# Performance work log

Hardware: AMD Instinct MI355X
Metric: run time of the kernel (lower is better)

Reference implementation:

```python
import jax, jax.numpy as jnp
import numpy as np


def setup_inputs() -> dict:
    key = jax.random.key(0)
    ks = jax.random.split(key, 13)
    B, W, C = 16, 2048, 512
    inp = {
        "X_sfr": jax.random.normal(ks[0], (B, W, C), dtype=jnp.float32),
        "adj_matrix": jax.random.normal(ks[1], (B, C, C), dtype=jnp.float32),
        "log_temp": jnp.zeros((1,), dtype=jnp.float32),
        "wq": jax.random.normal(ks[2], (1,), dtype=jnp.float32),
        "bq": jax.random.normal(ks[3], (1,), dtype=jnp.float32),
        "wk": jax.random.normal(ks[4], (1,), dtype=jnp.float32),
        "bk": jax.random.normal(ks[5], (1,), dtype=jnp.float32),
        "wv": jax.random.normal(ks[6], (1,), dtype=jnp.float32),
        "bv": jax.random.normal(ks[7], (1,), dtype=jnp.float32),
        "wmu": jax.random.normal(ks[8], (1,), dtype=jnp.float32),
        "bmu": jax.random.normal(ks[9], (1,), dtype=jnp.float32),
        "wsig": jax.random.normal(ks[10], (1,), dtype=jnp.float32),
        "bsig": jax.random.normal(ks[11], (1,), dtype=jnp.float32),
        "k1": 20,
        "k2": 30,
    }
    return inp


def reference(X_sfr, adj_matrix, log_temp, wq, bq, wk, bk, wv, bv, wmu, bmu, wsig, bsig, k1, k2):
    B, W, C = X_sfr.shape
    # spatial propagation: relu + in-degree normalize adjacency
    adj_nonneg = jnp.maximum(adj_matrix, 0.0)
    in_deg = jnp.clip(adj_nonneg.sum(axis=1, keepdims=True), 1e-4)  # [B,1,C]
    adj_norm = adj_nonneg / in_deg
    X_spatial = jnp.einsum('bwi,bij->bwj', X_sfr, adj_norm)  # [B,W,C]

    # static band mask over time: k1 <= |dt| <= k2, fallback to identity rows
    t = jnp.arange(W)
    delta = jnp.abs(t[None, :] - t[:, None])
    band = (delta >= k1) & (delta <= k2)  # [W,W]
    has_valid = band.any(axis=1)
    band = jnp.where(has_valid[:, None], band, jnp.eye(W, dtype=bool))

    # scalar (1->1) q/k/v projections on the temporal token
    temporal_token = X_spatial.mean(axis=2, keepdims=True)  # [B,W,1]
    q = wq * temporal_token + bq                            # [B,W,1]
    k = wk * temporal_token + bk                            # [B,W,1]
    v = wv * X_spatial + bv                                 # [B,W,C]

    temp = jax.nn.softplus(log_temp)[0] + 1e-4
    logits = jnp.matmul(q, jnp.swapaxes(k, 1, 2)) / temp    # [B,W,W] rank-1
    logits = jnp.where(band[None, :, :], logits, -1e9)
    attn = jax.nn.softmax(logits, axis=-1)
    attn = attn * band[None, :, :].astype(attn.dtype)
    attn = attn / (attn.sum(axis=-1, keepdims=True) + 1e-6)

    sacon_scalar = attn.sum(axis=-1, keepdims=True)         # [B,W,1]
    sacon = jnp.broadcast_to(sacon_scalar, (B, W, C))

    X_temporal = jnp.matmul(attn, v)                        # [B,W,C]
    X_fused = X_temporal + X_spatial

    mu = jnp.clip(wmu * X_fused + bmu, -20.0, 20.0)
    sigma_sq = jax.nn.softplus(wsig * X_fused + bsig) + 0.1
    return mu, sigma_sq, sacon
```

## Files before the change

kernel.cpp:

```cpp
#include <hip/hip_runtime.h>
#include <math.h>

#define B_ 16
#define W_ 2048
#define C_ 512

#define OFF_XB    0
#define OFF_BT    33554432
#define OFF_XSP   41943040
#define OFF_TT    75497472
#define OFF_CS    75628544

typedef short v8s __attribute__((ext_vector_type(8)));
typedef float v4f __attribute__((ext_vector_type(4)));
typedef float v2f __attribute__((ext_vector_type(2)));
typedef unsigned int u32;

__device__ __forceinline__ float softplus_fast(float x) {
    return fmaxf(x, 0.f) + __logf(1.f + __expf(-fabsf(x)));
}
__device__ __forceinline__ unsigned short f2bf(float x) {
    unsigned int u = __float_as_uint(x);
    unsigned int r = (u + 0x7FFFu + ((u >> 16) & 1u)) >> 16;
    return (unsigned short)r;
}
__device__ __forceinline__ float bf2f_lo(unsigned int u) {
    return __uint_as_float(u << 16);
}
__device__ __forceinline__ float bf2f_hi(unsigned int u) {
    return __uint_as_float(u & 0xffff0000u);
}
__device__ __forceinline__ void gload16(const ushort* g, ushort* l) {
    __builtin_amdgcn_global_load_lds(
        (const __attribute__((address_space(1))) u32*)(g),
        (__attribute__((address_space(3))) u32*)(l), 16, 0, 0);
}

__global__ __launch_bounds__(256) void front_k(const float* __restrict__ X,
                                               ushort* __restrict__ Xb,
                                               const float* __restrict__ adj,
                                               ushort* __restrict__ Bt,
                                               float* __restrict__ cs) {
    const int bid = blockIdx.x;
    if (bid < 4096) {
        const size_t e0 = ((size_t)bid * 256 + threadIdx.x) * 16;
        const float4* Xp = (const float4*)(X + e0);
        float4 a = Xp[0], b = Xp[1], c = Xp[2], d = Xp[3];
        v8s o0, o1;
        o0[0] = (short)f2bf(a.x); o0[1] = (short)f2bf(a.y);
        o0[2] = (short)f2bf(a.z); o0[3] = (short)f2bf(a.w);
        o0[4] = (short)f2bf(b.x); o0[5] = (short)f2bf(b.y);
        o0[6] = (short)f2bf(b.z); o0[7] = (short)f2bf(b.w);
        o1[0] = (short)f2bf(c.x); o1[1] = (short)f2bf(c.y);
        o1[2] = (short)f2bf(c.z); o1[3] = (short)f2bf(c.w);
        o1[4] = (short)f2bf(d.x); o1[5] = (short)f2bf(d.y);
        o1[6] = (short)f2bf(d.z); o1[7] = (short)f2bf(d.w);
        *(v8s*)&Xb[e0]     = o0;
        *(v8s*)&Xb[e0 + 8] = o1;
    } else {
        __shared__ float t[64][65];
        const int cb = bid - 4096;
        const int b  = cb >> 6;
        const int rem = cb & 63;
        const int i0 = (rem & 7) * 64;
        const int j0 = (rem >> 3) * 64;
        const int tid = threadIdx.x;
        const int tx = tid & 15, ty = tid >> 4;

#pragma unroll
        for (int p = 0; p < 4; p++) {
            const int iy = ty + p * 16;
            const float4 v = *(const float4*)&adj[((size_t)b * C_ + (i0 + iy)) * C_ + j0 + tx * 4];
            t[iy][tx * 4 + 0] = fmaxf(v.x, 0.f);
            t[iy][tx * 4 + 1] = fmaxf(v.y, 0.f);
            t[iy][tx * 4 + 2] = fmaxf(v.z, 0.f);
            t[iy][tx * 4 + 3] = fmaxf(v.w, 0.f);
        }
        __syncthreads();

        const int jj = tid >> 2;
        const int i4 = (tid & 3) * 16;
        float psum = 0.f;
        v8s o0, o1;
#pragma unroll
        for (int k = 0; k < 8; k++) {
            float v = t[i4 + k][jj];
            psum += v;
            o0[k] = (short)f2bf(v);
        }
#pragma unroll
        for (int k = 0; k < 8; k++) {
            float v = t[i4 + 8 + k][jj];
            psum += v;
            o1[k] = (short)f2bf(v);
        }
        ushort* dst = &Bt[(size_t)b * C_ * C_ + (size_t)(j0 + jj) * C_ + i0 + i4];
        *(v8s*)dst       = o0;
        *(v8s*)(dst + 8) = o1;
        psum += __shfl_xor(psum, 1);
        psum += __shfl_xor(psum, 2);
        if ((tid & 3) == 0) atomicAdd(&cs[b * C_ + j0 + jj], psum);
    }
}

__global__ __launch_bounds__(256) void gemm_mfma(const ushort* __restrict__ Xb,
                                                 const ushort* __restrict__ Bt,
                                                 const float* __restrict__ cs,
                                                 ushort* __restrict__ Xsp,
                                                 float* __restrict__ tt) {
    __shared__ ushort As[2][128 * 32];
    __shared__ ushort Bs[2][128 * 32];
    __shared__ float invL[128];
    const int b  = blockIdx.z;
    const int m0 = blockIdx.y * 128;
    const int n0 = blockIdx.x * 128;
    const int tid  = threadIdx.x;
    const int wave = tid >> 6, lane = tid & 63;
    const int quad = lane >> 4, l16 = lane & 15;
    const int mw = (wave & 1) * 64, nw = (wave >> 1) * 64;

    if (tid < 128) invL[tid] = 1.f / fmaxf(cs[b * C_ + n0 + tid], 1e-4f);

    const ushort* Ag = Xb + (size_t)b * W_ * C_ + (size_t)m0 * C_;
    const ushort* Bg = Bt + (size_t)b * C_ * C_ + (size_t)n0 * C_;

    const int sm = tid >> 2;
    const int sk = (tid & 3) * 8;

    v4f acc[4][4];
#pragma unroll
    for (int mt = 0; mt < 4; mt++)
#pragma unroll
        for (int nt = 0; nt < 4; nt++)
            acc[mt][nt] = (v4f){0.f, 0.f, 0.f, 0.f};

    for (int k0 = 0; k0 < C_; k0 += 64) {
        __syncthreads();
        gload16(Ag + (size_t)sm * C_ + k0 + sk,             &As[0][tid * 8]);
        gload16(Ag + (size_t)(sm + 64) * C_ + k0 + sk,      &As[0][2048 + tid * 8]);
        gload16(Bg + (size_t)sm * C_ + k0 + sk,             &Bs[0][tid * 8]);
        gload16(Bg + (size_t)(sm + 64) * C_ + k0 + sk,      &Bs[0][2048 + tid * 8]);
        gload16(Ag + (size_t)sm * C_ + k0 + 32 + sk,        &As[1][tid * 8]);
        gload16(Ag + (size_t)(sm + 64) * C_ + k0 + 32 + sk, &As[1][2048 + tid * 8]);
        gload16(Bg + (size_t)sm * C_ + k0 + 32 + sk,        &Bs[1][tid * 8]);
        gload16(Bg + (size_t)(sm + 64) * C_ + k0 + 32 + sk, &Bs[1][2048 + tid * 8]);
        __syncthreads();

#pragma unroll
        for (int h = 0; h < 2; h++) {
            v8s af[4], bf[4];
#pragma unroll
            for (int mt = 0; mt < 4; mt++)
                af[mt] = *(const v8s*)&As[h][(mw + mt * 16 + l16) * 32 + quad * 8];
#pragma unroll
            for (int nt = 0; nt < 4; nt++)
                bf[nt] = *(const v8s*)&Bs[h][(nw + nt * 16 + l16) * 32 + quad * 8];
#pragma unroll
            for (int mt = 0; mt < 4; mt++)
#pragma unroll
                for (int nt = 0; nt < 4; nt++)
                    acc[mt][nt] = __builtin_amdgcn_mfma_f32_16x16x32_bf16(bf[nt], af[mt], acc[mt][nt], 0, 0, 0);
        }
    }

#pragma unroll
    for (int nt = 0; nt < 4; nt++) {
        const v4f iv = *(const v4f*)&invL[nw + nt * 16 + quad * 4];
#pragma unroll
        for (int mt = 0; mt < 4; mt++)
#pragma unroll
            for (int r = 0; r < 4; r++)
                acc[mt][nt][r] *= iv[r];
    }

#pragma unroll
    for (int mt = 0; mt < 4; mt++) {
        const int row = m0 + mw + mt * 16 + l16;
        ushort* rowp = &Xsp[((size_t)b * W_ + row) * C_];
#pragma unroll
        for (int nt = 0; nt < 4; nt++) {
            const int colb = n0 + nw + nt * 16 + quad * 4;
            ushort4 o;
            o.x = f2bf(acc[mt][nt][0]);
            o.y = f2bf(acc[mt][nt][1]);
            o.z = f2bf(acc[mt][nt][2]);
            o.w = f2bf(acc[mt][nt][3]);
            *(ushort4*)&rowp[colb] = o;
        }
        float s = 0.f;
#pragma unroll
        for (int nt = 0; nt < 4; nt++)
#pragma unroll
            for (int r = 0; r < 4; r++) s += acc[mt][nt][r];
        s += __shfl_xor(s, 16);
        s += __shfl_xor(s, 32);
        if (quad == 0) atomicAdd(&tt[b * W_ + row], s);
    }
}

__global__ __launch_bounds__(256) void final_kernel(const ushort* __restrict__ Xsp,
                                                    const float* __restrict__ tt,
                                                    const float* __restrict__ ltp,
                                                    const float* __restrict__ wqp, const float* __restrict__ bqp,
                                                    const float* __restrict__ wkp, const float* __restrict__ bkp,
                                                    const float* __restrict__ wvp, const float* __restrict__ bvp,
                                                    const float* __restrict__ wmup, const float* __restrict__ bmup,
                                                    const float* __restrict__ wsigp, const float* __restrict__ bsigp,
                                                    const int* __restrict__ k1p, const int* __restrict__ k2p,
                                                    float* __restrict__ out) {
    __shared__ float wlds[4][40][4];
    const int wid = threadIdx.x >> 6, lane = threadIdx.x & 63;
    const int bid = ((int)blockIdx.x & 7) * 256 + ((int)blockIdx.x >> 3);
    const int i0w = bid * 16 + wid * 4;
    const int b = i0w >> 11, ib = i0w & (W_ - 1);
    const int K1 = k1p[0], K2 = k2p[0];
    int ns = K2 - K1 + 1;
    if (ns > 16) ns = 16;
    const int n2 = 2 * ns;
    const int nsL = ns + 3;
    const int nu = 2 * nsL;
    const float Sc = 1.f / (1.f + 1e-6f);

    for (int k = threadIdx.x; k < 4 * 40 * 4; k += 256) ((float*)wlds)[k] = 0.f;
    __syncthreads();

    {
        const float cinv = 1.f / C_;
        const float temp = softplus_fast(ltp[0]) + 1e-4f;
        const float invt = 1.f / temp;
        const float wkc = wkp[0] * cinv, bk = bkp[0];
        const float wqc = wqp[0] * cinv, bq = bqp[0];
        const float* ttb = tt + b * W_;
        const int half = lane >> 5;
        const int s = lane & 31;
#pragma unroll
        for (int rr = 0; rr < 2; rr++) {
            const int r = rr * 2 + half;
            const int i = ib + r;
            const float q = wqc * ttb[i] + bq;
            int j = (s < ns) ? (i - K2 + s) : (i + K1 + (s - ns));
            bool valid = (s < n2) && (j >= 0) && (j < W_);
            int jc = min(max(j, 0), W_ - 1);
            float l = valid ? (q * (wkc * ttb[jc] + bk) * invt) : -1e30f;
            float mx = l;
#pragma unroll
            for (int off = 16; off > 0; off >>= 1) mx = fmaxf(mx, __shfl_xor(mx, off, 32));
            float e = valid ? __expf(l - mx) : 0.f;
            float T = e;
#pragma unroll
            for (int off = 16; off > 0; off >>= 1) T += __shfl_xor(T, off, 32);
            float wsc = (1.f / T) * Sc;
            if (valid) {
                int u = (s < ns) ? (r + s) : (nsL + r + (s - ns));
                wlds[wid][u][r] = e * wsc;
            }
        }
    }
    __syncthreads();

    const ushort* Xbp = Xsp + (size_t)b * W_ * C_;
    const int c8 = lane * 8;

    uint4 xv[4];
#pragma unroll
    for (int r = 0; r < 4; r++)
        xv[r] = *(const uint4*)(Xbp + (size_t)(ib + r) * C_ + c8);

    v2f acc2[4][4];
#pragma unroll
    for (int r = 0; r < 4; r++)
#pragma unroll
        for (int p = 0; p < 4; p++) acc2[r][p] = (v2f){0.f, 0.f};

    auto band_addr = [&](int u) -> const uint4* {
        int j = (u < nsL) ? (ib - K2 + u) : (ib + K1 + (u - nsL));
        j = min(max(j, 0), W_ - 1);
        return (const uint4*)(Xbp + (size_t)j * C_ + c8);
    };
    uint4 vA = *band_addr(0);
    uint4 vB = *band_addr(1);
    for (int u = 0; u < nu; u++) {
        uint4 v = vA;
        vA = vB;
        if (u + 2 < nu) vB = *band_addr(u + 2);
        v2f x[4];
        x[0] = (v2f){bf2f_lo(v.x), bf2f_hi(v.x)};
        x[1] = (v2f){bf2f_lo(v.y), bf2f_hi(v.y)};
        x[2] = (v2f){bf2f_lo(v.z), bf2f_hi(v.z)};
        x[3] = (v2f){bf2f_lo(v.w), bf2f_hi(v.w)};
        const v4f w4 = *(const v4f*)&wlds[wid][u][0];
#pragma unroll
        for (int r = 0; r < 4; r++) {
            v2f w2 = (v2f){w4[r], w4[r]};
#pragma unroll
            for (int p = 0; p < 4; p++) acc2[r][p] += w2 * x[p];
        }
    }

    const float wv = wvp[0], bvS = bvp[0] * Sc;
    const float wmu = wmup[0], bmu = bmup[0];
    const float wsig = wsigp[0], bsig = bsigp[0];
    const size_t N = (size_t)B_ * W_ * C_;

#pragma unroll
    for (int r = 0; r < 4; r++) {
        float xs[8];
        xs[0] = bf2f_lo(xv[r].x); xs[1] = bf2f_hi(xv[r].x);
        xs[2] = bf2f_lo(xv[r].y); xs[3] = bf2f_hi(xv[r].y);
        xs[4] = bf2f_lo(xv[r].z); xs[5] = bf2f_hi(xv[r].z);
        xs[6] = bf2f_lo(xv[r].w); xs[7] = bf2f_hi(xv[r].w);

        float mu[8], sg[8];
#pragma unroll
        for (int k = 0; k < 8; k++) {
            float a = acc2[r][k >> 1][k & 1];
            float xf = fmaf(wv, a, bvS) + xs[k];
            mu[k] = fminf(fmaxf(fmaf(wmu, xf, bmu), -20.f), 20.f);
            sg[k] = softplus_fast(fmaf(wsig, xf, bsig)) + 0.1f;
        }

        const size_t base = (size_t)(i0w + r) * C_ + c8;
        __builtin_nontemporal_store((v4f){mu[0], mu[1], mu[2], mu[3]}, (v4f*)&out[base]);
        __builtin_nontemporal_store((v4f){mu[4], mu[5], mu[6], mu[7]}, (v4f*)&out[base + 4]);
        __builtin_nontemporal_store((v4f){sg[0], sg[1], sg[2], sg[3]}, (v4f*)&out[N + base]);
        __builtin_nontemporal_store((v4f){sg[4], sg[5], sg[6], sg[7]}, (v4f*)&out[N + base + 4]);
        __builtin_nontemporal_store((v4f){Sc, Sc, Sc, Sc}, (v4f*)&out[2 * N + base]);
        __builtin_nontemporal_store((v4f){Sc, Sc, Sc, Sc}, (v4f*)&out[2 * N + base + 4]);
    }
}

extern "C" void kernel_launch(void* const* d_in, const int* in_sizes, int n_in,
                              void* d_out, int out_size, void* d_ws, size_t ws_size,
                              hipStream_t stream) {
    const float* X_sfr = (const float*)d_in[0];
    const float* adj   = (const float*)d_in[1];
    const float* ltp   = (const float*)d_in[2];
    const float* wq    = (const float*)d_in[3];
    const float* bq    = (const float*)d_in[4];
    const float* wk    = (const float*)d_in[5];
    const float* bk    = (const float*)d_in[6];
    const float* wv    = (const float*)d_in[7];
    const float* bv    = (const float*)d_in[8];
    const float* wmu   = (const float*)d_in[9];
    const float* bmu   = (const float*)d_in[10];
    const float* wsig  = (const float*)d_in[11];
    const float* bsig  = (const float*)d_in[12];
    const int*   k1p   = (const int*)d_in[13];
    const int*   k2p   = (const int*)d_in[14];

    char* ws = (char*)d_ws;
    ushort* Xb  = (ushort*)(ws + OFF_XB);
    ushort* Bt  = (ushort*)(ws + OFF_BT);
    ushort* Xsp = (ushort*)(ws + OFF_XSP);
    float*  tt  = (float*)(ws + OFF_TT);
    float*  cs  = (float*)(ws + OFF_CS);
    float*  out = (float*)d_out;

    hipMemsetAsync(tt, 0, B_ * W_ * sizeof(float) + B_ * C_ * sizeof(float), stream);

    front_k<<<4096 + 1024, 256, 0, stream>>>(X_sfr, Xb, adj, Bt, cs);

    gemm_mfma<<<dim3(C_ / 128, W_ / 128, B_), 256, 0, stream>>>(Xb, Bt, cs, Xsp, tt);

    final_kernel<<<(B_ * W_) / 16, 256, 0, stream>>>(Xsp, tt, ltp, wq, bq, wk, bk,
                                                     wv, bv, wmu, bmu, wsig, bsig,
                                                     k1p, k2p, out);
}
```

Baseline: 395.0 us.

## Fuse fp32-to-bf16 conversion of X into GEMM A-tile loading and remap block order

The separate pass that converted X to bf16 in a workspace is removed. The GEMM now reads fp32 X directly, converts it in registers and writes bf16 into shared memory, which avoids one full write and re-read of a bf16 copy of X. A 1D grid with a swizzled block-to-tile mapping groups neighbouring M panels with all four N tiles, which should improve L2 reuse. The cost is that each GEMM block reads twice as many bytes for A, and those reads become synchronous register loads instead of async global-to-LDS loads, so latency hiding may suffer.

```diff
diff --git a/kernel.cpp b/kernel.cpp
--- a/kernel.cpp
+++ b/kernel.cpp
@@ -5,7 +5,6 @@
 #define W_ 2048
 #define C_ 512
 
-#define OFF_XB    0
 #define OFF_BT    33554432
 #define OFF_XSP   41943040
 #define OFF_TT    75497472
@@ -36,74 +35,54 @@
         (__attribute__((address_space(3))) u32*)(l), 16, 0, 0);
 }
 
-__global__ __launch_bounds__(256) void front_k(const float* __restrict__ X,
-                                               ushort* __restrict__ Xb,
-                                               const float* __restrict__ adj,
-                                               ushort* __restrict__ Bt,
-                                               float* __restrict__ cs) {
-    const int bid = blockIdx.x;
-    if (bid < 4096) {
-        const size_t e0 = ((size_t)bid * 256 + threadIdx.x) * 16;
-        const float4* Xp = (const float4*)(X + e0);
-        float4 a = Xp[0], b = Xp[1], c = Xp[2], d = Xp[3];
-        v8s o0, o1;
-        o0[0] = (short)f2bf(a.x); o0[1] = (short)f2bf(a.y);
-        o0[2] = (short)f2bf(a.z); o0[3] = (short)f2bf(a.w);
-        o0[4] = (short)f2bf(b.x); o0[5] = (short)f2bf(b.y);
-        o0[6] = (short)f2bf(b.z); o0[7] = (short)f2bf(b.w);
-        o1[0] = (short)f2bf(c.x); o1[1] = (short)f2bf(c.y);
-        o1[2] = (short)f2bf(c.z); o1[3] = (short)f2bf(c.w);
-        o1[4] = (short)f2bf(d.x); o1[5] = (short)f2bf(d.y);
-        o1[6] = (short)f2bf(d.z); o1[7] = (short)f2bf(d.w);
-        *(v8s*)&Xb[e0]     = o0;
-        *(v8s*)&Xb[e0 + 8] = o1;
-    } else {
-        __shared__ float t[64][65];
-        const int cb = bid - 4096;
-        const int b  = cb >> 6;
-        const int rem = cb & 63;
-        const int i0 = (rem & 7) * 64;
-        const int j0 = (rem >> 3) * 64;
-        const int tid = threadIdx.x;
-        const int tx = tid & 15, ty = tid >> 4;
-
-#pragma unroll
-        for (int p = 0; p < 4; p++) {
-            const int iy = ty + p * 16;
-            const float4 v = *(const float4*)&adj[((size_t)b * C_ + (i0 + iy)) * C_ + j0 + tx * 4];
-            t[iy][tx * 4 + 0] = fmaxf(v.x, 0.f);
-            t[iy][tx * 4 + 1] = fmaxf(v.y, 0.f);
-            t[iy][tx * 4 + 2] = fmaxf(v.z, 0.f);
-            t[iy][tx * 4 + 3] = fmaxf(v.w, 0.f);
-        }
-        __syncthreads();
-
-        const int jj = tid >> 2;
-        const int i4 = (tid & 3) * 16;
-        float psum = 0.f;
-        v8s o0, o1;
-#pragma unroll
-        for (int k = 0; k < 8; k++) {
-            float v = t[i4 + k][jj];
-            psum += v;
-            o0[k] = (short)f2bf(v);
-        }
-#pragma unroll
-        for (int k = 0; k < 8; k++) {
-            float v = t[i4 + 8 + k][jj];
-            psum += v;
-            o1[k] = (short)f2bf(v);
-        }
-        ushort* dst = &Bt[(size_t)b * C_ * C_ + (size_t)(j0 + jj) * C_ + i0 + i4];
-        *(v8s*)dst       = o0;
-        *(v8s*)(dst + 8) = o1;
-        psum += __shfl_xor(psum, 1);
-        psum += __shfl_xor(psum, 2);
-        if ((tid & 3) == 0) atomicAdd(&cs[b * C_ + j0 + jj], psum);
-    }
-}
-
-__global__ __launch_bounds__(256) void gemm_mfma(const ushort* __restrict__ Xb,
+__global__ __launch_bounds__(256) void adj_k(const float* __restrict__ adj,
+                                             ushort* __restrict__ Bt,
+                                             float* __restrict__ cs) {
+    __shared__ float t[64][65];
+    const int cb = blockIdx.x;
+    const int b  = cb >> 6;
+    const int rem = cb & 63;
+    const int i0 = (rem & 7) * 64;
+    const int j0 = (rem >> 3) * 64;
+    const int tid = threadIdx.x;
+    const int tx = tid & 15, ty = tid >> 4;
+
+#pragma unroll
+    for (int p = 0; p < 4; p++) {
+        const int iy = ty + p * 16;
+        const float4 v = *(const float4*)&adj[((size_t)b * C_ + (i0 + iy)) * C_ + j0 + tx * 4];
+        t[iy][tx * 4 + 0] = fmaxf(v.x, 0.f);
+        t[iy][tx * 4 + 1] = fmaxf(v.y, 0.f);
+        t[iy][tx * 4 + 2] = fmaxf(v.z, 0.f);
+        t[iy][tx * 4 + 3] = fmaxf(v.w, 0.f);
+    }
+    __syncthreads();
+
+    const int jj = tid >> 2;
+    const int i4 = (tid & 3) * 16;
+    float psum = 0.f;
+    v8s o0, o1;
+#pragma unroll
+    for (int k = 0; k < 8; k++) {
+        float v = t[i4 + k][jj];
+        psum += v;
+        o0[k] = (short)f2bf(v);
+    }
+#pragma unroll
+    for (int k = 0; k < 8; k++) {
+        float v = t[i4 + 8 + k][jj];
+        psum += v;
+        o1[k] = (short)f2bf(v);
+    }
+    ushort* dst = &Bt[(size_t)b * C_ * C_ + (size_t)(j0 + jj) * C_ + i0 + i4];
+    *(v8s*)dst       = o0;
+    *(v8s*)(dst + 8) = o1;
+    psum += __shfl_xor(psum, 1);
+    psum += __shfl_xor(psum, 2);
+    if ((tid & 3) == 0) atomicAdd(&cs[b * C_ + j0 + jj], psum);
+}
+
+__global__ __launch_bounds__(256) void gemm_mfma(const float* __restrict__ X,
                                                  const ushort* __restrict__ Bt,
                                                  const float* __restrict__ cs,
                                                  ushort* __restrict__ Xsp,
@@ -111,9 +90,14 @@
     __shared__ ushort As[2][128 * 32];
     __shared__ ushort Bs[2][128 * 32];
     __shared__ float invL[128];
-    const int b  = blockIdx.z;
-    const int m0 = blockIdx.y * 128;
-    const int n0 = blockIdx.x * 128;
+    const int id = blockIdx.x;
+    const int g  = id >> 5;
+    const int j  = id & 7;
+    const int n  = (id >> 3) & 3;
+    const int panel = (g << 3) + j;
+    const int b  = panel >> 4;
+    const int m0 = (panel & 15) * 128;
+    const int n0 = n * 128;
     const int tid  = threadIdx.x;
     const int wave = tid >> 6, lane = tid & 63;
     const int quad = lane >> 4, l16 = lane & 15;
@@ -121,11 +105,13 @@
 
     if (tid < 128) invL[tid] = 1.f / fmaxf(cs[b * C_ + n0 + tid], 1e-4f);
 
-    const ushort* Ag = Xb + (size_t)b * W_ * C_ + (size_t)m0 * C_;
+    const float*  Ag = X  + (size_t)b * W_ * C_ + (size_t)m0 * C_;
     const ushort* Bg = Bt + (size_t)b * C_ * C_ + (size_t)n0 * C_;
 
     const int sm = tid >> 2;
     const int sk = (tid & 3) * 8;
+    const int arow = tid >> 1;
+    const int ah   = tid & 1;
 
     v4f acc[4][4];
 #pragma unroll
@@ -136,14 +122,22 @@
 
     for (int k0 = 0; k0 < C_; k0 += 64) {
         __syncthreads();
-        gload16(Ag + (size_t)sm * C_ + k0 + sk,             &As[0][tid * 8]);
-        gload16(Ag + (size_t)(sm + 64) * C_ + k0 + sk,      &As[0][2048 + tid * 8]);
         gload16(Bg + (size_t)sm * C_ + k0 + sk,             &Bs[0][tid * 8]);
         gload16(Bg + (size_t)(sm + 64) * C_ + k0 + sk,      &Bs[0][2048 + tid * 8]);
-        gload16(Ag + (size_t)sm * C_ + k0 + 32 + sk,        &As[1][tid * 8]);
-        gload16(Ag + (size_t)(sm + 64) * C_ + k0 + 32 + sk, &As[1][2048 + tid * 8]);
         gload16(Bg + (size_t)sm * C_ + k0 + 32 + sk,        &Bs[1][tid * 8]);
         gload16(Bg + (size_t)(sm + 64) * C_ + k0 + 32 + sk, &Bs[1][2048 + tid * 8]);
+        const float* ap = Ag + (size_t)arow * C_ + k0 + ah * 32;
+#pragma unroll
+        for (int cc = 0; cc < 4; cc++) {
+            const float4 f0 = *(const float4*)(ap + cc * 8);
+            const float4 f1 = *(const float4*)(ap + cc * 8 + 4);
+            v8s o;
+            o[0] = (short)f2bf(f0.x); o[1] = (short)f2bf(f0.y);
+            o[2] = (short)f2bf(f0.z); o[3] = (short)f2bf(f0.w);
+            o[4] = (short)f2bf(f1.x); o[5] = (short)f2bf(f1.y);
+            o[6] = (short)f2bf(f1.z); o[7] = (short)f2bf(f1.w);
+            *(v8s*)&As[ah][arow * 32 + cc * 8] = o;
+        }
         __syncthreads();
 
 #pragma unroll
@@ -349,7 +343,6 @@
     const int*   k2p   = (const int*)d_in[14];
 
     char* ws = (char*)d_ws;
-    ushort* Xb  = (ushort*)(ws + OFF_XB);
     ushort* Bt  = (ushort*)(ws + OFF_BT);
     ushort* Xsp = (ushort*)(ws + OFF_XSP);
     float*  tt  = (float*)(ws + OFF_TT);
@@ -358,9 +351,9 @@
 
     hipMemsetAsync(tt, 0, B_ * W_ * sizeof(float) + B_ * C_ * sizeof(float), stream);
 
-    front_k<<<4096 + 1024, 256, 0, stream>>>(X_sfr, Xb, adj, Bt, cs);
-
-    gemm_mfma<<<dim3(C_ / 128, W_ / 128, B_), 256, 0, stream>>>(Xb, Bt, cs, Xsp, tt);
+    adj_k<<<1024, 256, 0, stream>>>(adj, Bt, cs);
+
+    gemm_mfma<<<1024, 256, 0, stream>>>(X_sfr, Bt, cs, Xsp, tt);
 
     final_kernel<<<(B_ * W_) / 16, 256, 0, stream>>>(Xsp, tt, ltp, wq, bq, wk, bk,
                                                      wv, bv, wmu, bmu, wsig, bsig,
```

After: 404.0 us. 1.02x slower.
